# Kernel optimization log

Hardware: AMD Instinct MI355X
Metric: run time of the kernel (lower is better)

The kernel has to match this reference:

```python
import jax, jax.numpy as jnp
import numpy as np

TAU, RHO, OFFSET, DELTA, START = 0.01, 100.0, 1.44, 0.05, 0.5
N_LEVELS = 3


def _heaviside(x):
    # torch.heaviside(x, values=1.0): 0 for x<0, 1 for x==0, 1 for x>0
    return jnp.where(x < 0, 0.0, 1.0).astype(x.dtype)


def _tau_sigmoid(x, tau):
    # 1 / (1 + exp(clamp(-x/tau, -50, 50)))
    e = jnp.clip(-x / tau, -50.0, 50.0)
    return 1.0 / (1.0 + jnp.exp(e))


def _step_rank(x, target):
    # x: [B, B, B] score diffs; target: [B, B] int relevance counts
    # inferior_relevance[b, i, j] = target[b, i] > target[b, j]
    inferior = target[:, :, None] > target[:, None, :]
    pos = x > 0
    margin = x > DELTA
    sig = _tau_sigmoid(x, TAU)
    pos_branch = jnp.where(margin, RHO * (x - DELTA) + OFFSET, START + sig)
    inf_val = jnp.where(pos, pos_branch, sig)
    return jnp.where(inferior, inf_val, _heaviside(x))


def setup_inputs() -> dict:
    key = jax.random.key(0)
    k1, k2 = jax.random.split(key)
    B, D = 384, 512
    emb = jax.random.normal(k1, (B, D), dtype=jnp.float32)
    emb = emb / jnp.linalg.norm(emb, axis=-1, keepdims=True)  # cosine-sim embeddings
    labels = jax.random.randint(k2, (B, N_LEVELS), 0, 8, dtype=jnp.int64)
    return {"embeddings": emb, "labels": labels}


def reference(embeddings, labels):
    B = embeddings.shape[0]
    scores = embeddings @ embeddings.T                      # [B, B]
    # create_label_matrix: count of matching hierarchy levels
    target = (labels[:, None, :] == labels[None, :, :]).sum(-1)  # [B, B] int
    relevances = target.astype(scores.dtype) / N_LEVELS          # [B, B]

    mask = 1.0 - jnp.eye(B, dtype=scores.dtype)             # [B, B] (broadcast over batch)
    # sim_diff[b, i, j] = scores[b, j] - scores[b, i]
    sim_diff = scores[:, None, :] - scores[:, :, None]      # [B, B, B]
    min_rel = jnp.minimum(relevances[:, :, None], relevances[:, None, :])

    rank = 1.0 + jnp.sum(_step_rank(sim_diff, target) * mask, axis=-1)      # [B, B]
    hrank = relevances + jnp.sum(_heaviside(sim_diff) * min_rel * mask, axis=-1)

    mhap = (hrank / rank).sum(-1) / relevances.sum(-1)      # [B]
    return jnp.mean(1.0 - mhap)                             # return_type='1-mHAP', reduce='mean'
```

## Files before the change

kernel.cpp:

```cpp
#include <hip/hip_runtime.h>
#include <hip/hip_bf16.h>

#define NB 384
#define ND 512

__global__ __launch_bounds__(256) void gemm_scores(const float* __restrict__ emb,
                                                   float* __restrict__ s0,
                                                   float* __restrict__ s1) {
    __shared__ float As[32][65];
    __shared__ float Bs[32][65];
    const int tid = threadIdx.x;
    const int tx = tid & 15, ty = tid >> 4;
    const int i0 = blockIdx.y * 32, j0 = blockIdx.x * 32;
    const int kbase = blockIdx.z * (ND / 2);
    float* __restrict__ s = blockIdx.z ? s1 : s0;
    float acc00 = 0.f, acc01 = 0.f, acc10 = 0.f, acc11 = 0.f;

    for (int k0 = kbase; k0 < kbase + ND / 2; k0 += 64) {
#pragma unroll
        for (int p = 0; p < 2; ++p) {
            int idx = tid + 256 * p;
            int r = idx >> 4;
            int c = (idx & 15) << 2;
            float4 av = *reinterpret_cast<const float4*>(emb + (i0 + r) * ND + k0 + c);
            As[r][c] = av.x; As[r][c + 1] = av.y; As[r][c + 2] = av.z; As[r][c + 3] = av.w;
            float4 bv = *reinterpret_cast<const float4*>(emb + (j0 + r) * ND + k0 + c);
            Bs[r][c] = bv.x; Bs[r][c + 1] = bv.y; Bs[r][c + 2] = bv.z; Bs[r][c + 3] = bv.w;
        }
        __syncthreads();
#pragma unroll 8
        for (int kk = 0; kk < 64; ++kk) {
            float a0 = As[2 * ty][kk], a1 = As[2 * ty + 1][kk];
            float b0 = Bs[2 * tx][kk], b1 = Bs[2 * tx + 1][kk];
            acc00 = fmaf(a0, b0, acc00); acc01 = fmaf(a0, b1, acc01);
            acc10 = fmaf(a1, b0, acc10); acc11 = fmaf(a1, b1, acc11);
        }
        __syncthreads();
    }
    const int i = i0 + 2 * ty, j = j0 + 2 * tx;
    s[i * NB + j]           = acc00; s[i * NB + j + 1]       = acc01;
    s[(i + 1) * NB + j]     = acc10; s[(i + 1) * NB + j + 1] = acc11;
}

__global__ __launch_bounds__(NB) void hap_prep(const float* __restrict__ s0,
                                               const float* __restrict__ s1,
                                               const int* __restrict__ labels,
                                               float* __restrict__ g,
                                               int* __restrict__ offs,
                                               float* __restrict__ tsumArr) {
    __shared__ int wcnt[6][4];
    __shared__ int wbase[6][4];
    __shared__ int cbase[4];
    const int tid = threadIdx.x, lane = tid & 63, wv = tid >> 6;
    const int b = blockIdx.x;
    const int l0 = labels[b * 3 + 0], l1 = labels[b * 3 + 1], l2 = labels[b * 3 + 2];
    const int t = (labels[tid * 3 + 0] == l0) + (labels[tid * 3 + 1] == l1) +
                  (labels[tid * 3 + 2] == l2);
    const float sv = s0[b * NB + tid] + s1[b * NB + tid];
    const unsigned long long mlt = (1ull << lane) - 1ull;
    int myrank = 0;
#pragma unroll
    for (int c = 0; c < 4; ++c) {
        unsigned long long m = __ballot(t == c);
        if (t == c) myrank = __popcll(m & mlt);
        if (lane == 0) wcnt[wv][c] = __popcll(m);
    }
    __syncthreads();
    if (tid == 0) {
        int tot0 = 0, tot1 = 0, tot2 = 0, tot3 = 0;
        for (int w = 0; w < 6; ++w) {
            wbase[w][0] = tot0; tot0 += wcnt[w][0];
            wbase[w][1] = tot1; tot1 += wcnt[w][1];
            wbase[w][2] = tot2; tot2 += wcnt[w][2];
            wbase[w][3] = tot3; tot3 += wcnt[w][3];
        }
        cbase[0] = 0; cbase[1] = tot0; cbase[2] = tot0 + tot1; cbase[3] = tot0 + tot1 + tot2;
        offs[b * 4 + 0] = cbase[1];
        offs[b * 4 + 1] = cbase[2];
        offs[b * 4 + 2] = cbase[3];
        tsumArr[b] = (float)(tot1 + 2 * tot2 + 3 * tot3);
    }
    __syncthreads();
    g[b * NB + cbase[t] + wbase[wv][t] + myrank] = sv;
}

__global__ __launch_bounds__(192) void hap_part(const float* __restrict__ g,
                                                const int* __restrict__ offs,
                                                float2* __restrict__ part) {
    __shared__ alignas(16) float gs[192];
    const int tid = threadIdx.x;
    const int b = blockIdx.x, ih = blockIdx.y, jh = blockIdx.z;
    const int w0 = jh * 192;

    gs[tid] = g[b * NB + w0 + tid];
    const int i = ih * 192 + tid;
    const float si = g[b * NB + i];
    const int S1 = offs[b * 4 + 0], S2 = offs[b * 4 + 1], S3 = offs[b * 4 + 2];
    const int ti = (i >= S1) + (i >= S2) + (i >= S3);
    __syncthreads();

    const int R[5] = {0, S1, S2, S3, NB};
    const float siK = si * -144.26950408889634f;
    const float pconst = fmaf(-100.f, si, -3.56f);
    const float c1 = si + 0.05f;

    float rsum = 0.f, hsum = 0.f;
#pragma unroll
    for (int c = 0; c < 4; ++c) {
        int lo = (R[c] > w0 ? R[c] : w0) - w0;
        int hi = (R[c + 1] < w0 + 192 ? R[c + 1] : w0 + 192) - w0;
        if (lo >= hi) continue;
        if (ti > c) {
            float rs = 0.f; int cnt = 0;
#pragma unroll 2
            for (int k = lo; k < hi; ++k) {
                const float sj = gs[k];
                const float ex = __builtin_amdgcn_exp2f(fmaf(sj, -144.26950408889634f, -siK));
                const float sg = __builtin_amdgcn_rcpf(1.f + ex);
                const float posb = fmaf(100.f, sj, pconst);
                const float sel = (sj > c1) ? posb : (0.5f + sg);
                rs += (sj > si) ? sel : sg;
                cnt += (sj >= si);
            }
            rsum += rs; hsum += (float)(c * cnt);
        } else {
            int cnt = 0;
            int k = lo;
            for (; k < hi && (k & 3); ++k) cnt += (gs[k] >= si);
            for (; k + 4 <= hi; k += 4) {
                const float4 v = *reinterpret_cast<const float4*>(&gs[k]);
                cnt += (v.x >= si) + (v.y >= si) + (v.z >= si) + (v.w >= si);
            }
            for (; k < hi; ++k) cnt += (gs[k] >= si);
            rsum += (float)cnt; hsum += (float)(ti * cnt);
        }
    }
    part[jh * (NB * NB) + b * NB + i] = make_float2(rsum, hsum);
}

__global__ __launch_bounds__(192) void hap_combine(const float2* __restrict__ part,
                                                   const float* __restrict__ tsumArr,
                                                   float* __restrict__ bsum) {
    __shared__ float redQ[3];
    const int tid = threadIdx.x, lane = tid & 63, wv = tid >> 6;
    const int b = blockIdx.x;
    float q = 0.f;
#pragma unroll
    for (int rep = 0; rep < 2; ++rep) {
        const int i = rep * 192 + tid;
        const float2 p0 = part[b * NB + i];
        const float2 p1 = part[NB * NB + b * NB + i];
        q += (p0.y + p1.y) / (p0.x + p1.x);
    }
#pragma unroll
    for (int off = 32; off > 0; off >>= 1) q += __shfl_xor(q, off, 64);
    if (lane == 0) redQ[wv] = q;
    __syncthreads();
    if (tid == 0) bsum[b] = (redQ[0] + redQ[1] + redQ[2]) / (tsumArr[b] * (float)NB);
}

__global__ __launch_bounds__(64) void hap_final(const float* __restrict__ bsum,
                                                float* __restrict__ out) {
    const int tid = threadIdx.x;
    float p = 0.f;
    for (int k = tid; k < NB; k += 64) p += bsum[k];
#pragma unroll
    for (int off = 32; off > 0; off >>= 1) p += __shfl_xor(p, off, 64);
    if (tid == 0) out[0] = 1.f - p;
}

extern "C" void kernel_launch(void* const* d_in, const int* in_sizes, int n_in,
                              void* d_out, int out_size, void* d_ws, size_t ws_size,
                              hipStream_t stream) {
    const float* emb = (const float*)d_in[0];
    const int* labels = (const int*)d_in[1];
    float* out = (float*)d_out;

    float* s0 = (float*)d_ws;
    float* s1 = s0 + NB * NB;
    float* g  = s1 + NB * NB;
    float2* part = (float2*)(g + NB * NB);
    int* offs = (int*)(part + 2 * NB * NB);
    float* tsumArr = (float*)(offs + NB * 4);
    float* bsum = tsumArr + NB;

    gemm_scores<<<dim3(12, 12, 2), 256, 0, stream>>>(emb, s0, s1);
    hap_prep<<<NB, NB, 0, stream>>>(s0, s1, labels, g, offs, tsumArr);
    hap_part<<<dim3(NB, 2, 2), 192, 0, stream>>>(g, offs, part);
    hap_combine<<<NB, 192, 0, stream>>>(part, tsumArr, bsum);
    hap_final<<<1, 64, 0, stream>>>(bsum, out);
}
```

Before: 44.80 us.

## Fuse prep, partial and combine kernels into one per-row HAP kernel

Merges the bucket-sort prep, pairwise partial-sum and combine kernels into a single kernel. Each block recomputes the relevance sort of its row into shared memory and processes half of the i indices over the full j range. This drops two launches and the global round trips for the sorted scores, offsets and partial sums. The trade-offs are that the sort is done twice per row, the grid shrinks from 4 to 2 blocks per row, and per-thread work doubles, which may lengthen the critical path.

```diff
diff --git a/kernel.cpp b/kernel.cpp
--- a/kernel.cpp
+++ b/kernel.cpp
@@ -42,28 +42,55 @@
     s[(i + 1) * NB + j]     = acc10; s[(i + 1) * NB + j + 1] = acc11;
 }
 
-__global__ __launch_bounds__(NB) void hap_prep(const float* __restrict__ s0,
-                                               const float* __restrict__ s1,
-                                               const int* __restrict__ labels,
-                                               float* __restrict__ g,
-                                               int* __restrict__ offs,
-                                               float* __restrict__ tsumArr) {
+template <bool NEED_CNT>
+__device__ __forceinline__ void sig_run(const float* __restrict__ gs, int lo, int hi,
+                                        float si, float siK, float pconst, float c1,
+                                        float& rsum, int& cnt) {
+#pragma unroll 2
+    for (int k = lo; k < hi; ++k) {
+        const float sj = gs[k];
+        const float ex = __builtin_amdgcn_exp2f(fmaf(sj, -144.26950408889634f, -siK));
+        const float sg = __builtin_amdgcn_rcpf(1.f + ex);
+        const float posb = fmaf(100.f, sj, pconst);
+        const float sel = (sj > c1) ? posb : (0.5f + sg);
+        rsum += (sj > si) ? sel : sg;
+        if (NEED_CNT) cnt += (sj >= si);
+    }
+}
+
+__global__ __launch_bounds__(192) void hap_fused(const float* __restrict__ s0,
+                                                 const float* __restrict__ s1,
+                                                 const int* __restrict__ labels,
+                                                 float* __restrict__ bpart) {
+    __shared__ alignas(16) float gs[NB];
     __shared__ int wcnt[6][4];
     __shared__ int wbase[6][4];
-    __shared__ int cbase[4];
+    __shared__ int cbase[5];
+    __shared__ float tsum_sh;
+    __shared__ float redQ[3];
+
     const int tid = threadIdx.x, lane = tid & 63, wv = tid >> 6;
-    const int b = blockIdx.x;
+    const int b = blockIdx.x, ih = blockIdx.y;
+
     const int l0 = labels[b * 3 + 0], l1 = labels[b * 3 + 1], l2 = labels[b * 3 + 2];
-    const int t = (labels[tid * 3 + 0] == l0) + (labels[tid * 3 + 1] == l1) +
-                  (labels[tid * 3 + 2] == l2);
-    const float sv = s0[b * NB + tid] + s1[b * NB + tid];
+
+    const int jA = tid, jB = tid + 192;
+    const int tA = (labels[jA * 3 + 0] == l0) + (labels[jA * 3 + 1] == l1) +
+                   (labels[jA * 3 + 2] == l2);
+    const int tB = (labels[jB * 3 + 0] == l0) + (labels[jB * 3 + 1] == l1) +
+                   (labels[jB * 3 + 2] == l2);
+    const float svA = s0[b * NB + jA] + s1[b * NB + jA];
+    const float svB = s0[b * NB + jB] + s1[b * NB + jB];
+
     const unsigned long long mlt = (1ull << lane) - 1ull;
-    int myrank = 0;
+    int rkA = 0, rkB = 0;
 #pragma unroll
     for (int c = 0; c < 4; ++c) {
-        unsigned long long m = __ballot(t == c);
-        if (t == c) myrank = __popcll(m & mlt);
-        if (lane == 0) wcnt[wv][c] = __popcll(m);
+        unsigned long long mA = __ballot(tA == c);
+        unsigned long long mB = __ballot(tB == c);
+        if (tA == c) rkA = __popcll(mA & mlt);
+        if (tB == c) rkB = __popcll(mB & mlt);
+        if (lane == 0) { wcnt[wv][c] = __popcll(mA); wcnt[3 + wv][c] = __popcll(mB); }
     }
     __syncthreads();
     if (tid == 0) {
@@ -74,96 +101,64 @@
             wbase[w][2] = tot2; tot2 += wcnt[w][2];
             wbase[w][3] = tot3; tot3 += wcnt[w][3];
         }
-        cbase[0] = 0; cbase[1] = tot0; cbase[2] = tot0 + tot1; cbase[3] = tot0 + tot1 + tot2;
-        offs[b * 4 + 0] = cbase[1];
-        offs[b * 4 + 1] = cbase[2];
-        offs[b * 4 + 2] = cbase[3];
-        tsumArr[b] = (float)(tot1 + 2 * tot2 + 3 * tot3);
+        cbase[0] = 0; cbase[1] = tot0; cbase[2] = tot0 + tot1;
+        cbase[3] = tot0 + tot1 + tot2; cbase[4] = NB;
+        tsum_sh = (float)(tot1 + 2 * tot2 + 3 * tot3);
     }
     __syncthreads();
-    g[b * NB + cbase[t] + wbase[wv][t] + myrank] = sv;
-}
-
-__global__ __launch_bounds__(192) void hap_part(const float* __restrict__ g,
-                                                const int* __restrict__ offs,
-                                                float2* __restrict__ part) {
-    __shared__ alignas(16) float gs[192];
-    const int tid = threadIdx.x;
-    const int b = blockIdx.x, ih = blockIdx.y, jh = blockIdx.z;
-    const int w0 = jh * 192;
-
-    gs[tid] = g[b * NB + w0 + tid];
-    const int i = ih * 192 + tid;
-    const float si = g[b * NB + i];
-    const int S1 = offs[b * 4 + 0], S2 = offs[b * 4 + 1], S3 = offs[b * 4 + 2];
-    const int ti = (i >= S1) + (i >= S2) + (i >= S3);
+    gs[cbase[tA] + wbase[wv][tA] + rkA] = svA;
+    gs[cbase[tB] + wbase[3 + wv][tB] + rkB] = svB;
     __syncthreads();
 
-    const int R[5] = {0, S1, S2, S3, NB};
+    const int S1 = cbase[1], S2 = cbase[2], S3 = cbase[3];
+    const int i = ih * 192 + tid;
+    const float si = gs[i];
+    const int ti = (i >= S1) + (i >= S2) + (i >= S3);
     const float siK = si * -144.26950408889634f;
     const float pconst = fmaf(-100.f, si, -3.56f);
     const float c1 = si + 0.05f;
 
     float rsum = 0.f, hsum = 0.f;
-#pragma unroll
-    for (int c = 0; c < 4; ++c) {
-        int lo = (R[c] > w0 ? R[c] : w0) - w0;
-        int hi = (R[c + 1] < w0 + 192 ? R[c + 1] : w0 + 192) - w0;
-        if (lo >= hi) continue;
-        if (ti > c) {
-            float rs = 0.f; int cnt = 0;
-#pragma unroll 2
-            for (int k = lo; k < hi; ++k) {
-                const float sj = gs[k];
-                const float ex = __builtin_amdgcn_exp2f(fmaf(sj, -144.26950408889634f, -siK));
-                const float sg = __builtin_amdgcn_rcpf(1.f + ex);
-                const float posb = fmaf(100.f, sj, pconst);
-                const float sel = (sj > c1) ? posb : (0.5f + sg);
-                rs += (sj > si) ? sel : sg;
-                cnt += (sj >= si);
-            }
-            rsum += rs; hsum += (float)(c * cnt);
-        } else {
-            int cnt = 0;
-            int k = lo;
-            for (; k < hi && (k & 3); ++k) cnt += (gs[k] >= si);
-            for (; k + 4 <= hi; k += 4) {
-                const float4 v = *reinterpret_cast<const float4*>(&gs[k]);
-                cnt += (v.x >= si) + (v.y >= si) + (v.z >= si) + (v.w >= si);
-            }
-            for (; k < hi; ++k) cnt += (gs[k] >= si);
-            rsum += (float)cnt; hsum += (float)(ti * cnt);
+    int cnt = 0;
+    if (ti > 0) {
+        sig_run<false>(gs, 0, S1, si, siK, pconst, c1, rsum, cnt);
+    }
+    if (ti > 1) {
+        int c1n = 0;
+        sig_run<true>(gs, S1, S2, si, siK, pconst, c1, rsum, c1n);
+        hsum += (float)c1n;
+    }
+    if (ti > 2) {
+        int c2n = 0;
+        sig_run<true>(gs, S2, S3, si, siK, pconst, c1, rsum, c2n);
+        hsum += (float)(2 * c2n);
+    }
+    {
+        const int lo = cbase[ti];
+        int k = lo, hcnt = 0;
+        for (; k < NB && (k & 3); ++k) hcnt += (gs[k] >= si);
+        for (; k + 4 <= NB; k += 4) {
+            const float4 v = *reinterpret_cast<const float4*>(&gs[k]);
+            hcnt += (v.x >= si) + (v.y >= si) + (v.z >= si) + (v.w >= si);
         }
+        rsum += (float)hcnt;
+        hsum += (float)(ti * hcnt);
     }
-    part[jh * (NB * NB) + b * NB + i] = make_float2(rsum, hsum);
-}
 
-__global__ __launch_bounds__(192) void hap_combine(const float2* __restrict__ part,
-                                                   const float* __restrict__ tsumArr,
-                                                   float* __restrict__ bsum) {
-    __shared__ float redQ[3];
-    const int tid = threadIdx.x, lane = tid & 63, wv = tid >> 6;
-    const int b = blockIdx.x;
-    float q = 0.f;
-#pragma unroll
-    for (int rep = 0; rep < 2; ++rep) {
-        const int i = rep * 192 + tid;
-        const float2 p0 = part[b * NB + i];
-        const float2 p1 = part[NB * NB + b * NB + i];
-        q += (p0.y + p1.y) / (p0.x + p1.x);
-    }
+    float q = hsum / rsum;
 #pragma unroll
     for (int off = 32; off > 0; off >>= 1) q += __shfl_xor(q, off, 64);
     if (lane == 0) redQ[wv] = q;
     __syncthreads();
-    if (tid == 0) bsum[b] = (redQ[0] + redQ[1] + redQ[2]) / (tsumArr[b] * (float)NB);
+    if (tid == 0)
+        bpart[b * 2 + ih] = (redQ[0] + redQ[1] + redQ[2]) / (tsum_sh * (float)NB);
 }
 
-__global__ __launch_bounds__(64) void hap_final(const float* __restrict__ bsum,
+__global__ __launch_bounds__(64) void hap_final(const float* __restrict__ bpart,
                                                 float* __restrict__ out) {
     const int tid = threadIdx.x;
     float p = 0.f;
-    for (int k = tid; k < NB; k += 64) p += bsum[k];
+    for (int k = tid; k < NB * 2; k += 64) p += bpart[k];
 #pragma unroll
     for (int off = 32; off > 0; off >>= 1) p += __shfl_xor(p, off, 64);
     if (tid == 0) out[0] = 1.f - p;
@@ -178,15 +173,9 @@
 
     float* s0 = (float*)d_ws;
     float* s1 = s0 + NB * NB;
-    float* g  = s1 + NB * NB;
-    float2* part = (float2*)(g + NB * NB);
-    int* offs = (int*)(part + 2 * NB * NB);
-    float* tsumArr = (float*)(offs + NB * 4);
-    float* bsum = tsumArr + NB;
+    float* bpart = s1 + NB * NB;
 
     gemm_scores<<<dim3(12, 12, 2), 256, 0, stream>>>(emb, s0, s1);
-    hap_prep<<<NB, NB, 0, stream>>>(s0, s1, labels, g, offs, tsumArr);
-    hap_part<<<dim3(NB, 2, 2), 192, 0, stream>>>(g, offs, part);
-    hap_combine<<<NB, 192, 0, stream>>>(part, tsumArr, bsum);
-    hap_final<<<1, 64, 0, stream>>>(bsum, out);
+    hap_fused<<<dim3(NB, 2), 192, 0, stream>>>(s0, s1, labels, bpart);
+    hap_final<<<1, 64, 0, stream>>>(bpart, out);
 }
```

After: 44.31 us. Within noise of the previous version (-1.1%).

## Split hap_part j-range into four chunks and flatten per-class loop

Applied to the files above, without the earlier changes.

The j dimension of the pairwise pass is split into four 96-wide chunks instead of two 192-wide ones, doubling the block count to improve load balance and occupancy. Because the columns are sorted by relevance class, the per-class loop becomes a single prefix loop over the lower-class columns (sigmoid path, with the hierarchical weight computed per column) followed by a plain count loop. The combine kernel now sums four partials per row, which adds workspace traffic.

```diff
diff --git a/kernel.cpp b/kernel.cpp
--- a/kernel.cpp
+++ b/kernel.cpp
@@ -87,55 +87,46 @@
 __global__ __launch_bounds__(192) void hap_part(const float* __restrict__ g,
                                                 const int* __restrict__ offs,
                                                 float2* __restrict__ part) {
-    __shared__ alignas(16) float gs[192];
+    __shared__ alignas(16) float gs[96];
     const int tid = threadIdx.x;
     const int b = blockIdx.x, ih = blockIdx.y, jh = blockIdx.z;
-    const int w0 = jh * 192;
+    const int q0 = jh * 96;
 
-    gs[tid] = g[b * NB + w0 + tid];
+    if (tid < 96) gs[tid] = g[b * NB + q0 + tid];
     const int i = ih * 192 + tid;
     const float si = g[b * NB + i];
     const int S1 = offs[b * 4 + 0], S2 = offs[b * 4 + 1], S3 = offs[b * 4 + 2];
     const int ti = (i >= S1) + (i >= S2) + (i >= S3);
     __syncthreads();
 
-    const int R[5] = {0, S1, S2, S3, NB};
-    const float siK = si * -144.26950408889634f;
+    const int Rti = (ti == 0) ? 0 : (ti == 1) ? S1 : (ti == 2) ? S2 : S3;
+    int m = Rti - q0; m = m < 0 ? 0 : (m > 96 ? 96 : m);
+
+    const float nsiK = si * 144.26950408889634f;
     const float pconst = fmaf(-100.f, si, -3.56f);
     const float c1 = si + 0.05f;
 
-    float rsum = 0.f, hsum = 0.f;
-#pragma unroll
-    for (int c = 0; c < 4; ++c) {
-        int lo = (R[c] > w0 ? R[c] : w0) - w0;
-        int hi = (R[c + 1] < w0 + 192 ? R[c + 1] : w0 + 192) - w0;
-        if (lo >= hi) continue;
-        if (ti > c) {
-            float rs = 0.f; int cnt = 0;
-#pragma unroll 2
-            for (int k = lo; k < hi; ++k) {
-                const float sj = gs[k];
-                const float ex = __builtin_amdgcn_exp2f(fmaf(sj, -144.26950408889634f, -siK));
-                const float sg = __builtin_amdgcn_rcpf(1.f + ex);
-                const float posb = fmaf(100.f, sj, pconst);
-                const float sel = (sj > c1) ? posb : (0.5f + sg);
-                rs += (sj > si) ? sel : sg;
-                cnt += (sj >= si);
-            }
-            rsum += rs; hsum += (float)(c * cnt);
-        } else {
-            int cnt = 0;
-            int k = lo;
-            for (; k < hi && (k & 3); ++k) cnt += (gs[k] >= si);
-            for (; k + 4 <= hi; k += 4) {
-                const float4 v = *reinterpret_cast<const float4*>(&gs[k]);
-                cnt += (v.x >= si) + (v.y >= si) + (v.z >= si) + (v.w >= si);
-            }
-            for (; k < hi; ++k) cnt += (gs[k] >= si);
-            rsum += (float)cnt; hsum += (float)(ti * cnt);
-        }
+    float rs = 0.f, hs = 0.f;
+    int k = 0;
+#pragma unroll 4
+    for (; k < m; ++k) {
+        const float sj = gs[k];
+        const float ex = __builtin_amdgcn_exp2f(fmaf(sj, -144.26950408889634f, nsiK));
+        const float sg = __builtin_amdgcn_rcpf(1.f + ex);
+        const float posb = fmaf(100.f, sj, pconst);
+        const float sel = (sj > c1) ? posb : (0.5f + sg);
+        rs += (sj > si) ? sel : sg;
+        const int pos = q0 + k;
+        const float wk = (float)((pos >= S1) + (pos >= S2));
+        hs += (sj >= si) ? wk : 0.f;
     }
-    part[jh * (NB * NB) + b * NB + i] = make_float2(rsum, hsum);
+    int cnt = 0;
+#pragma unroll 8
+    for (; k < 96; ++k) cnt += (gs[k] >= si) ? 1 : 0;
+
+    rs += (float)cnt;
+    hs += (float)(ti * cnt);
+    part[(jh * NB + b) * NB + i] = make_float2(rs, hs);
 }
 
 __global__ __launch_bounds__(192) void hap_combine(const float2* __restrict__ part,
@@ -148,9 +139,13 @@
 #pragma unroll
     for (int rep = 0; rep < 2; ++rep) {
         const int i = rep * 192 + tid;
-        const float2 p0 = part[b * NB + i];
-        const float2 p1 = part[NB * NB + b * NB + i];
-        q += (p0.y + p1.y) / (p0.x + p1.x);
+        float r = 0.f, h = 0.f;
+#pragma unroll
+        for (int jh = 0; jh < 4; ++jh) {
+            const float2 p = part[(jh * NB + b) * NB + i];
+            r += p.x; h += p.y;
+        }
+        q += h / r;
     }
 #pragma unroll
     for (int off = 32; off > 0; off >>= 1) q += __shfl_xor(q, off, 64);
@@ -180,13 +175,13 @@
     float* s1 = s0 + NB * NB;
     float* g  = s1 + NB * NB;
     float2* part = (float2*)(g + NB * NB);
-    int* offs = (int*)(part + 2 * NB * NB);
+    int* offs = (int*)(part + 4 * NB * NB);
     float* tsumArr = (float*)(offs + NB * 4);
     float* bsum = tsumArr + NB;
 
     gemm_scores<<<dim3(12, 12, 2), 256, 0, stream>>>(emb, s0, s1);
     hap_prep<<<NB, NB, 0, stream>>>(s0, s1, labels, g, offs, tsumArr);
-    hap_part<<<dim3(NB, 2, 2), 192, 0, stream>>>(g, offs, part);
+    hap_part<<<dim3(NB, 2, 4), 192, 0, stream>>>(g, offs, part);
     hap_combine<<<NB, 192, 0, stream>>>(part, tsumArr, bsum);
     hap_final<<<1, 64, 0, stream>>>(bsum, out);
 }
```

New measurement: 46.06 us. 2.8% more time.
